# Kernel tuning notes

Hardware: AMD Instinct MI355X
Metric: run time of the kernel (lower is better)

## Reference

```python
import jax, jax.numpy as jnp
import numpy as np

D = 1536; H = 12; DH = 128; B = 1; S_TXT = 512; S_IMG = 1024; S = S_TXT + S_IMG; FF = 4 * D
EPS = 1e-6


def setup_inputs() -> dict:
    key = jax.random.key(0)
    ks = iter(jax.random.split(key, 64))
    def nrm(shape, s=1.0):
        return jax.random.normal(next(ks), shape, jnp.float32) * s
    w = 0.02
    inp = {}
    inp["hidden_states"] = nrm((B, S_IMG, D))
    inp["encoder_hidden_states"] = nrm((B, S_TXT, D))
    inp["temb"] = nrm((B, D))
    ang = jax.random.uniform(next(ks), (B, S, DH // 2), jnp.float32, 0.0, 2.0 * np.pi)
    c, s = jnp.cos(ang), jnp.sin(ang)
    rot = jnp.stack([jnp.stack([c, -s], -1), jnp.stack([s, c], -1)], -2)  # [B,S,DH/2,2,2]
    inp["image_rotary_emb"] = rot.reshape(1, 1, B * S, DH // 2, 2, 2)
    inp["adaln_img_w"] = nrm((D, 6 * D), w); inp["adaln_img_b"] = jnp.zeros((6 * D,), jnp.float32)
    inp["adaln_txt_w"] = nrm((D, 6 * D), w); inp["adaln_txt_b"] = jnp.zeros((6 * D,), jnp.float32)
    inp["qkv_img_w"] = nrm((D, 3 * D), w); inp["qkv_img_b"] = jnp.zeros((3 * D,), jnp.float32)
    inp["qkv_txt_w"] = nrm((D, 3 * D), w); inp["qkv_txt_b"] = jnp.zeros((3 * D,), jnp.float32)
    inp["q_norm_img"] = jnp.ones((DH,), jnp.float32); inp["k_norm_img"] = jnp.ones((DH,), jnp.float32)
    inp["q_norm_txt"] = jnp.ones((DH,), jnp.float32); inp["k_norm_txt"] = jnp.ones((DH,), jnp.float32)
    inp["out_img_w"] = nrm((D, D), w); inp["out_img_b"] = jnp.zeros((D,), jnp.float32)
    inp["out_txt_w"] = nrm((D, D), w); inp["out_txt_b"] = jnp.zeros((D,), jnp.float32)
    inp["mlp_img_w1"] = nrm((D, FF), w); inp["mlp_img_b1"] = jnp.zeros((FF,), jnp.float32)
    inp["mlp_img_w2"] = nrm((FF, D), w); inp["mlp_img_b2"] = jnp.zeros((D,), jnp.float32)
    inp["mlp_txt_w1"] = nrm((D, FF), w); inp["mlp_txt_b1"] = jnp.zeros((FF,), jnp.float32)
    inp["mlp_txt_w2"] = nrm((FF, D), w); inp["mlp_txt_b2"] = jnp.zeros((D,), jnp.float32)
    return inp


def _ln(x):  # LayerNorm, no affine
    m = jnp.mean(x, -1, keepdims=True)
    v = jnp.mean(jnp.square(x - m), -1, keepdims=True)
    return (x - m) * jax.lax.rsqrt(v + EPS)


def _rms(x, w):  # per-head RMSNorm
    return x * jax.lax.rsqrt(jnp.mean(jnp.square(x), -1, keepdims=True) + EPS) * w


def _rope(x, rot):  # x [B,H,S,DH], rot [B,S,DH/2,2,2]
    xp = x.reshape(*x.shape[:-1], DH // 2, 2)
    out = jnp.einsum('bsdij,bhsdj->bhsdi', rot, xp)
    return out.reshape(x.shape)


def _qkv(x, w, b, qn, kn):  # -> q,k,v each [B,H,S,DH]
    bb, ss, _ = x.shape
    qkv = (x @ w + b).reshape(bb, ss, 3, H, DH).transpose(2, 0, 3, 1, 4)
    q, k, v = qkv[0], qkv[1], qkv[2]
    return _rms(q, qn), _rms(k, kn), v


def _block(hidden_states, encoder_hidden_states, temb, rot,
           adaln_img_w, adaln_img_b, adaln_txt_w, adaln_txt_b,
           qkv_img_w, qkv_img_b, qkv_txt_w, qkv_txt_b,
           q_norm_img, k_norm_img, q_norm_txt, k_norm_txt,
           out_img_w, out_img_b, out_txt_w, out_txt_b,
           mlp_img_w1, mlp_img_b1, mlp_img_w2, mlp_img_b2,
           mlp_txt_w1, mlp_txt_b1, mlp_txt_w2, mlp_txt_b2):
    bsz = hidden_states.shape[0]
    s_txt = encoder_hidden_states.shape[1]
    t = jax.nn.silu(temb)
    emb_i = t @ adaln_img_w + adaln_img_b
    emb_t = t @ adaln_txt_w + adaln_txt_b
    sh_i, sc_i, g_i, shm_i, scm_i, gm_i = [e[:, None, :] for e in jnp.split(emb_i, 6, -1)]
    sh_t, sc_t, g_t, shm_t, scm_t, gm_t = [e[:, None, :] for e in jnp.split(emb_t, 6, -1)]

    n_img = _ln(hidden_states) * (1.0 + sc_i) + sh_i
    n_txt = _ln(encoder_hidden_states) * (1.0 + sc_t) + sh_t

    qi, ki, vi = _qkv(n_img, qkv_img_w, qkv_img_b, q_norm_img, k_norm_img)
    qt, kt, vt = _qkv(n_txt, qkv_txt_w, qkv_txt_b, q_norm_txt, k_norm_txt)
    q = jnp.concatenate([qt, qi], axis=2)
    k = jnp.concatenate([kt, ki], axis=2)
    v = jnp.concatenate([vt, vi], axis=2)

    rot = rot.reshape(bsz, q.shape[2], DH // 2, 2, 2)
    q = _rope(q, rot)
    k = _rope(k, rot)

    scale = 1.0 / np.sqrt(DH)
    attn = jax.nn.softmax(jnp.einsum('bhqd,bhkd->bhqk', q, k) * scale, axis=-1)
    o = jnp.einsum('bhqk,bhkd->bhqd', attn, v)          # [B,H,S,DH]
    o = o.transpose(0, 2, 1, 3).reshape(bsz, -1, D)     # [B,S,D]
    a_txt, a_img = o[:, :s_txt], o[:, s_txt:]

    hidden_states = hidden_states + g_i * (a_img @ out_img_w + out_img_b)
    encoder_hidden_states = encoder_hidden_states + g_t * (a_txt @ out_txt_w + out_txt_b)

    n2_img = _ln(hidden_states) * (1.0 + scm_i) + shm_i
    ff_img = jax.nn.gelu(n2_img @ mlp_img_w1 + mlp_img_b1, approximate=True) @ mlp_img_w2 + mlp_img_b2
    hidden_states = hidden_states + gm_i * ff_img

    n2_txt = _ln(encoder_hidden_states) * (1.0 + scm_t) + shm_t
    ff_txt = jax.nn.gelu(n2_txt @ mlp_txt_w1 + mlp_txt_b1, approximate=True) @ mlp_txt_w2 + mlp_txt_b2
    encoder_hidden_states = encoder_hidden_states + gm_t * ff_txt

    return jnp.concatenate([encoder_hidden_states, hidden_states], axis=1)


def reference(hidden_states, encoder_hidden_states, temb, image_rotary_emb,
              adaln_img_w, adaln_img_b, adaln_txt_w, adaln_txt_b,
              qkv_img_w, qkv_img_b, qkv_txt_w, qkv_txt_b,
              q_norm_img, k_norm_img, q_norm_txt, k_norm_txt,
              out_img_w, out_img_b, out_txt_w, out_txt_b,
              mlp_img_w1, mlp_img_b1, mlp_img_w2, mlp_img_b2,
              mlp_txt_w1, mlp_txt_b1, mlp_txt_w2, mlp_txt_b2):
    s_txt = encoder_hidden_states.shape[1]
    out = _block(hidden_states, encoder_hidden_states, temb, image_rotary_emb,
                 adaln_img_w, adaln_img_b, adaln_txt_w, adaln_txt_b,
                 qkv_img_w, qkv_img_b, qkv_txt_w, qkv_txt_b,
                 q_norm_img, k_norm_img, q_norm_txt, k_norm_txt,
                 out_img_w, out_img_b, out_txt_w, out_txt_b,
                 mlp_img_w1, mlp_img_b1, mlp_img_w2, mlp_img_b2,
                 mlp_txt_w1, mlp_txt_b1, mlp_txt_w2, mlp_txt_b2)
    return (out[:, :s_txt], out[:, s_txt:])
```

## Files before the change

kernel.cpp:

```cpp
#include <hip/hip_runtime.h>
#include <hip/hip_bf16.h>

typedef __bf16 bf16_t;
typedef __attribute__((ext_vector_type(4))) float f32x4;
typedef __attribute__((ext_vector_type(8))) bf16_t bf16x8;
typedef __attribute__((ext_vector_type(4))) bf16_t bf16x4;
typedef __attribute__((ext_vector_type(2))) bf16_t bf16x2;

#define D_MODEL 1536
#define NH 12
#define DHD 128
#define S_TXT 512
#define S_TOT 1536
#define FF_DIM 6144
#define KVSPLIT 4
#define HQB 288

__device__ inline bf16x8 ld_frag(const bf16_t* p) {
    bf16x4 a = *(const bf16x4*)p;
    bf16x4 b = *(const bf16x4*)(p + 16);
    bf16x8 r;
    r[0]=a[0]; r[1]=a[1]; r[2]=a[2]; r[3]=a[3];
    r[4]=b[0]; r[5]=b[1]; r[6]=b[2]; r[7]=b[3];
    return r;
}

__device__ inline void gload16(const void* g, void* l) {
    __builtin_amdgcn_global_load_lds((const __attribute__((address_space(1))) unsigned int*)g,
                                     (__attribute__((address_space(3))) unsigned int*)l, 16, 0, 0);
}

__global__ __launch_bounds__(256)
void adaln_p(const float* __restrict__ temb,
             const float* __restrict__ w_img, const float* __restrict__ w_txt,
             float* __restrict__ part) {
    __shared__ float t[192];
    int tid = threadIdx.x;
    int k0 = blockIdx.y * 192;
    if (tid < 192) {
        float x = temb[k0 + tid];
        t[tid] = x / (1.0f + __expf(-x));
    }
    __syncthreads();
    int n_g = blockIdx.x * 256 + tid;
    bool img = n_g < 9216;
    const float* W = img ? w_img : w_txt;
    int n = img ? n_g : n_g - 9216;
    float acc = 0.f;
    for (int kk = 0; kk < 192; kk += 4) {
        acc += t[kk]     * W[(size_t)(k0 + kk) * 9216 + n];
        acc += t[kk + 1] * W[(size_t)(k0 + kk + 1) * 9216 + n];
        acc += t[kk + 2] * W[(size_t)(k0 + kk + 2) * 9216 + n];
        acc += t[kk + 3] * W[(size_t)(k0 + kk + 3) * 9216 + n];
    }
    part[(size_t)blockIdx.y * 18432 + n_g] = acc;
}

__global__ __launch_bounds__(256)
void adaln_r(const float* __restrict__ part,
             const float* __restrict__ b_img, const float* __restrict__ b_txt,
             float* __restrict__ emb_img, float* __restrict__ emb_txt) {
    int n_g = blockIdx.x * 256 + threadIdx.x;
    float a = 0.f;
#pragma unroll
    for (int kc = 0; kc < 8; ++kc) a += part[(size_t)kc * 18432 + n_g];
    if (n_g < 9216) emb_img[n_g] = a + b_img[n_g];
    else            emb_txt[n_g - 9216] = a + b_txt[n_g - 9216];
}

__global__ __launch_bounds__(256)
void ln_mod(const float* __restrict__ src_txt, const float* __restrict__ src_img,
            const float* __restrict__ emb_t, const float* __restrict__ emb_i,
            int sh_c, int sc_c, bf16_t* __restrict__ out) {
    int row = blockIdx.x;
    bool txt = row < S_TXT;
    const float* src = txt ? src_txt + (size_t)row * D_MODEL
                           : src_img + (size_t)(row - S_TXT) * D_MODEL;
    const float* emb = txt ? emb_t : emb_i;
    int tid = threadIdx.x;
    float2 v[3];
    float s = 0.f, sq = 0.f;
#pragma unroll
    for (int i = 0; i < 3; ++i) {
        v[i] = *(const float2*)(src + tid * 2 + 512 * i);
        s  += v[i].x + v[i].y;
        sq += v[i].x * v[i].x + v[i].y * v[i].y;
    }
#pragma unroll
    for (int off = 32; off > 0; off >>= 1) {
        s  += __shfl_down(s, off);
        sq += __shfl_down(sq, off);
    }
    __shared__ float red[8];
    int wave = tid >> 6, lane = tid & 63;
    if (lane == 0) { red[wave] = s; red[4 + wave] = sq; }
    __syncthreads();
    float ts = red[0] + red[1] + red[2] + red[3];
    float tq = red[4] + red[5] + red[6] + red[7];
    float mean = ts * (1.0f / D_MODEL);
    float var  = tq * (1.0f / D_MODEL) - mean * mean;
    float rstd = rsqrtf(var + 1e-6f);
    bf16_t* op = out + (size_t)row * D_MODEL;
#pragma unroll
    for (int i = 0; i < 3; ++i) {
        int c0 = tid * 2 + 512 * i;
        bf16x2 r;
        r[0] = (bf16_t)((v[i].x - mean) * rstd * (1.0f + emb[sc_c * D_MODEL + c0])     + emb[sh_c * D_MODEL + c0]);
        r[1] = (bf16_t)((v[i].y - mean) * rstd * (1.0f + emb[sc_c * D_MODEL + c0 + 1]) + emb[sh_c * D_MODEL + c0 + 1]);
        *(bf16x2*)(op + c0) = r;
    }
}

template <int K, int N>
__global__ __launch_bounds__(256)
void conv_wt(const float* __restrict__ w_t, const float* __restrict__ w_i,
             bf16_t* __restrict__ dst) {
    __shared__ float tile[64][65];
    const float* src = blockIdx.z ? w_i : w_t;
    bf16_t* d = dst + (size_t)blockIdx.z * N * K;
    int bn = blockIdx.x * 64, bk = blockIdx.y * 64;
    int tid = threadIdx.x;
#pragma unroll
    for (int j = 0; j < 16; ++j) {
        int l = tid + 256 * j;
        int k = l >> 6, n = l & 63;
        tile[k][n] = src[(size_t)(bk + k) * N + bn + n];
    }
    __syncthreads();
#pragma unroll
    for (int j = 0; j < 16; ++j) {
        int l = tid + 256 * j;
        int n = l >> 6, k = l & 63;
        d[(size_t)(bn + n) * K + bk + k] = (bf16_t)tile[k][n];
    }
}

template <int EPI, typename OutT>
__global__ __launch_bounds__(256)
void gemm2(const bf16_t* __restrict__ A, int lda,
           const bf16_t* __restrict__ Wt, int wimg_off,
           const float* __restrict__ bias_t, const float* __restrict__ bias_i,
           const float* __restrict__ resid_t, const float* __restrict__ resid_i, int ldr,
           const float* __restrict__ gate_t, const float* __restrict__ gate_i,
           OutT* __restrict__ out, int ldo, int K) {
    __shared__ bf16_t As[2][128 * 64];
    __shared__ bf16_t Bs[2][128 * 64];
    const int tid = threadIdx.x;

    const int nbx = gridDim.x;
    const int nwg = nbx * gridDim.y;
    int lb = blockIdx.y * nbx + blockIdx.x;
    if ((nwg & 7) == 0) lb = (lb & 7) * (nwg >> 3) + (lb >> 3);
    const int bm = (lb / nbx) * 128, bn = (lb % nbx) * 128;

    const bool txt = bm < S_TXT;
    const bf16_t* W = txt ? Wt : Wt + wimg_off;
    const float* bias = txt ? bias_t : bias_i;
    const int wave = tid >> 6, lane = tid & 63;
    const int wr = (wave >> 1) * 64, wc = (wave & 1) * 64;
    const int lr = lane & 15, lg = lane >> 4;

    const int srow = wave * 8 + (lane >> 3);
    const int csrc = ((lane & 7) ^ ((lane >> 3) & 7)) * 8;
    const bf16_t* Ab = A + (size_t)(bm + srow) * lda + csrc;
    const bf16_t* Wb = W + (size_t)(bn + srow) * K + csrc;
    const int ldst = (wave * 8) * 64;

    f32x4 acc[4][4] = {};
    const int nt = K >> 6;

    auto stage = [&](int buf, int t) {
#pragma unroll
        for (int j = 0; j < 4; ++j) {
            gload16(Ab + (size_t)j * 32 * lda + t * 64, &As[buf][ldst + j * 2048]);
            gload16(Wb + (size_t)j * 32 * K   + t * 64, &Bs[buf][ldst + j * 2048]);
        }
    };

    stage(0, 0);
    asm volatile("s_waitcnt vmcnt(0)" ::: "memory");
    __builtin_amdgcn_s_barrier();

    int cur = 0;
    for (int t = 0; t < nt; ++t) {
        if (t + 1 < nt) stage(cur ^ 1, t + 1);
#pragma unroll
        for (int kk = 0; kk < 2; ++kk) {
            bf16x8 af[4], bfm[4];
#pragma unroll
            for (int m = 0; m < 4; ++m) {
                int rr = wr + m * 16 + lr;
                af[m] = *(const bf16x8*)&As[cur][rr * 64 + (((kk * 4 + lg) ^ (lr & 7)) * 8)];
            }
#pragma unroll
            for (int n = 0; n < 4; ++n) {
                int rr = wc + n * 16 + lr;
                bfm[n] = *(const bf16x8*)&Bs[cur][rr * 64 + (((kk * 4 + lg) ^ (lr & 7)) * 8)];
            }
#pragma unroll
            for (int m = 0; m < 4; ++m)
#pragma unroll
                for (int n = 0; n < 4; ++n)
                    acc[m][n] = __builtin_amdgcn_mfma_f32_16x16x32_bf16(af[m], bfm[n], acc[m][n], 0, 0, 0);
        }
        asm volatile("s_waitcnt vmcnt(0)" ::: "memory");
        __builtin_amdgcn_s_barrier();
        cur ^= 1;
    }

    const float* gate  = txt ? gate_t : gate_i;
    const float* resid = txt ? resid_t : resid_i;
    const int rbase = txt ? 0 : S_TXT;
#pragma unroll
    for (int m = 0; m < 4; ++m) {
#pragma unroll
        for (int r = 0; r < 4; ++r) {
            int grow = bm + wr + m * 16 + lg * 4 + r;
#pragma unroll
            for (int n = 0; n < 4; ++n) {
                int gcol = bn + wc + n * 16 + lr;
                float v = acc[m][n][r] + bias[gcol];
                if constexpr (EPI == 1) {
                    float x = v;
                    float th = tanhf(0.7978845608028654f * (x + 0.044715f * x * x * x));
                    v = 0.5f * x * (1.0f + th);
                } else if constexpr (EPI == 2) {
                    v = resid[(size_t)(grow - rbase) * ldr + gcol] + gate[gcol] * v;
                }
                out[(size_t)grow * ldo + gcol] = (OutT)v;
            }
        }
    }
}

__global__ __launch_bounds__(256)
void gemm3(const bf16_t* __restrict__ A, int lda,
           const bf16_t* __restrict__ Wt, int wimg_off,
           const float* __restrict__ bias_t, const float* __restrict__ bias_i,
           const float* __restrict__ resid_t, const float* __restrict__ resid_i, int ldr,
           const float* __restrict__ gate_t, const float* __restrict__ gate_i,
           float* __restrict__ out, int ldo, int K) {
    __shared__ bf16_t As[2][128 * 64];
    __shared__ bf16_t Bs[2][64 * 64];
    const int tid = threadIdx.x;

    const int nbx = gridDim.x;
    const int nwg = nbx * gridDim.y;
    int lb = blockIdx.y * nbx + blockIdx.x;
    if ((nwg & 7) == 0) lb = (lb & 7) * (nwg >> 3) + (lb >> 3);
    const int bm = (lb / nbx) * 128, bn = (lb % nbx) * 64;

    const bool txt = bm < S_TXT;
    const bf16_t* W = txt ? Wt : Wt + wimg_off;
    const float* bias = txt ? bias_t : bias_i;
    const int wave = tid >> 6, lane = tid & 63;
    const int wr = (wave >> 1) * 64, wc = (wave & 1) * 32;
    const int lr = lane & 15, lg = lane >> 4;

    const int srow = wave * 8 + (lane >> 3);
    const int csrc = ((lane & 7) ^ ((lane >> 3) & 7)) * 8;
    const bf16_t* Ab = A + (size_t)(bm + srow) * lda + csrc;
    const bf16_t* Wb = W + (size_t)(bn + srow) * K + csrc;
    const int ldst = (wave * 8) * 64;

    f32x4 acc[4][2] = {};
    const int nt = K >> 6;

    auto stage = [&](int buf, int t) {
#pragma unroll
        for (int j = 0; j < 4; ++j)
            gload16(Ab + (size_t)j * 32 * lda + t * 64, &As[buf][ldst + j * 2048]);
#pragma unroll
        for (int j = 0; j < 2; ++j)
            gload16(Wb + (size_t)j * 32 * K + t * 64, &Bs[buf][ldst + j * 2048]);
    };

    stage(0, 0);
    asm volatile("s_waitcnt vmcnt(0)" ::: "memory");
    __builtin_amdgcn_s_barrier();

    int cur = 0;
    for (int t = 0; t < nt; ++t) {
        if (t + 1 < nt) stage(cur ^ 1, t + 1);
#pragma unroll
        for (int kk = 0; kk < 2; ++kk) {
            bf16x8 af[4], bfm[2];
#pragma unroll
            for (int m = 0; m < 4; ++m) {
                int rr = wr + m * 16 + lr;
                af[m] = *(const bf16x8*)&As[cur][rr * 64 + (((kk * 4 + lg) ^ (lr & 7)) * 8)];
            }
#pragma unroll
            for (int n = 0; n < 2; ++n) {
                int rr = wc + n * 16 + lr;
                bfm[n] = *(const bf16x8*)&Bs[cur][rr * 64 + (((kk * 4 + lg) ^ (lr & 7)) * 8)];
            }
#pragma unroll
            for (int m = 0; m < 4; ++m)
#pragma unroll
                for (int n = 0; n < 2; ++n)
                    acc[m][n] = __builtin_amdgcn_mfma_f32_16x16x32_bf16(af[m], bfm[n], acc[m][n], 0, 0, 0);
        }
        asm volatile("s_waitcnt vmcnt(0)" ::: "memory");
        __builtin_amdgcn_s_barrier();
        cur ^= 1;
    }

    const float* gate  = txt ? gate_t : gate_i;
    const float* resid = txt ? resid_t : resid_i;
    const int rbase = txt ? 0 : S_TXT;
#pragma unroll
    for (int m = 0; m < 4; ++m) {
#pragma unroll
        for (int r = 0; r < 4; ++r) {
            int grow = bm + wr + m * 16 + lg * 4 + r;
#pragma unroll
            for (int n = 0; n < 2; ++n) {
                int gcol = bn + wc + n * 16 + lr;
                float v = acc[m][n][r] + bias[gcol];
                v = resid[(size_t)(grow - rbase) * ldr + gcol] + gate[gcol] * v;
                out[(size_t)grow * ldo + gcol] = v;
            }
        }
    }
}

__global__ __launch_bounds__(128)
void qkv_epi(const bf16_t* __restrict__ qkv, const float* __restrict__ rope,
             const float* __restrict__ qn_i, const float* __restrict__ kn_i,
             const float* __restrict__ qn_t, const float* __restrict__ kn_t,
             bf16_t* __restrict__ qb, bf16_t* __restrict__ kb) {
    int h = blockIdx.x, s = blockIdx.y, dh = threadIdx.x;
    bool txt = s < S_TXT;
    const float* qn = txt ? qn_t : qn_i;
    const float* kn = txt ? kn_t : kn_i;
    const bf16_t* base = qkv + (size_t)s * 4608 + h * DHD + dh;
    float q = (float)base[0];
    float k = (float)base[D_MODEL];
    float qs = q * q, ks = k * k;
#pragma unroll
    for (int off = 32; off > 0; off >>= 1) {
        qs += __shfl_down(qs, off);
        ks += __shfl_down(ks, off);
    }
    __shared__ float red[4];
    if ((threadIdx.x & 63) == 0) {
        red[(threadIdx.x >> 6) * 2]     = qs;
        red[(threadIdx.x >> 6) * 2 + 1] = ks;
    }
    __syncthreads();
    float qr = rsqrtf((red[0] + red[2]) * (1.0f / DHD) + 1e-6f);
    float kr = rsqrtf((red[1] + red[3]) * (1.0f / DHD) + 1e-6f);
    q = q * qr * qn[dh];
    k = k * kr * kn[dh];
    int i = dh & 1, d = dh >> 1;
    const float* rp = rope + ((size_t)s * 64 + d) * 4 + i * 2;
    float r0 = rp[0], r1 = rp[1];
    float qo = __shfl_xor(q, 1), ko = __shfl_xor(k, 1);
    float q0 = i ? qo : q, q1 = i ? q : qo;
    float k0 = i ? ko : k, k1 = i ? k : ko;
    float qq = r0 * q0 + r1 * q1;
    float kk = r0 * k0 + r1 * k1;
    size_t idx = ((size_t)h * S_TOT + s) * DHD + dh;
    qb[idx] = (bf16_t)(qq * 0.08838834764831845f);
    kb[idx] = (bf16_t)kk;
}

__global__ __launch_bounds__(256)
void v_tr(const bf16_t* __restrict__ qkv, bf16_t* __restrict__ vt) {
    __shared__ bf16_t tile[64][130];
    int h = blockIdx.x, sb = blockIdx.y * 64;
    int tid = threadIdx.x;
#pragma unroll
    for (int j = 0; j < 32; ++j) {
        int linear = tid + 256 * j;
        int sl = linear >> 7, dh = linear & 127;
        tile[sl][dh] = qkv[(size_t)(sb + sl) * 4608 + 2 * D_MODEL + h * DHD + dh];
    }
    __syncthreads();
#pragma unroll
    for (int j = 0; j < 32; ++j) {
        int linear = tid + 256 * j;
        int dh = linear >> 6, sl = linear & 63;
        vt[((size_t)h * DHD + dh) * S_TOT + sb + sl] = tile[sl][dh];
    }
}

__global__ __launch_bounds__(256)
void attn_k(const bf16_t* __restrict__ qbuf, const bf16_t* __restrict__ kbuf,
            const bf16_t* __restrict__ vt,
            float* __restrict__ part_o, float* __restrict__ part_ml) {
    __shared__ bf16_t Ks[2][64 * 128];
    __shared__ bf16_t Vs[2][128 * 64];
    __shared__ bf16_t P[4][16 * 64];
    int h = blockIdx.x, qblk = blockIdx.y, z = blockIdx.z;
    int q0 = qblk * 64;
    int tid = threadIdx.x, wave = tid >> 6, lane = tid & 63;
    int lr = lane & 15, lg = lane >> 4;

    const bf16_t* Qp = qbuf + ((size_t)h * S_TOT + q0 + wave * 16 + lr) * DHD;
    bf16x8 qf[4];
#pragma unroll
    for (int kk = 0; kk < 4; ++kk) qf[kk] = *(const bf16x8*)(Qp + (kk * 4 + lg) * 8);

    const int sKr = wave * 4 + (lane >> 4);
    const int cK = lane & 15;
    const bf16_t* Kb = kbuf + ((size_t)h * S_TOT + sKr) * DHD + ((cK ^ (sKr & 7)) * 8);
    const int ldsK = sKr * 128 - (lane >> 4) * 128 + 0;
    const int sVr = wave * 8 + (lane >> 3);
    const int cV = lane & 7;
    const bf16_t* Vb = vt + ((size_t)h * DHD + sVr) * S_TOT + ((cV ^ (sVr & 7)) * 8);
    const int ldsV = (wave * 8) * 64;

    auto stage = [&](int buf, int kb0) {
#pragma unroll
        for (int j = 0; j < 4; ++j) {
            gload16(Kb + (size_t)(kb0 + j * 16) * DHD, &Ks[buf][(wave * 4) * 128 + j * 2048]);
            gload16(Vb + kb0 + (size_t)j * 32 * S_TOT, &Vs[buf][ldsV + j * 2048]);
        }
    };

    f32x4 of[8] = {};
    float m[4] = {-1e30f, -1e30f, -1e30f, -1e30f};
    float l[4] = {};
    const int kv0 = z * (S_TOT / KVSPLIT);
    const int nt = (S_TOT / KVSPLIT) / 64;

    stage(0, kv0);
    asm volatile("s_waitcnt vmcnt(0)" ::: "memory");
    __builtin_amdgcn_s_barrier();

    int cur = 0;
    for (int t = 0; t < nt; ++t) {
        if (t + 1 < nt) stage(cur ^ 1, kv0 + (t + 1) * 64);
        f32x4 sf[4] = {};
        __builtin_amdgcn_s_setprio(1);
#pragma unroll
        for (int n = 0; n < 4; ++n) {
#pragma unroll
            for (int kk = 0; kk < 4; ++kk) {
                bf16x8 kf = *(const bf16x8*)&Ks[cur][(n * 16 + lr) * 128 + (((kk * 4 + lg) ^ (lr & 7)) * 8)];
                sf[n] = __builtin_amdgcn_mfma_f32_16x16x32_bf16(qf[kk], kf, sf[n], 0, 0, 0);
            }
        }
        __builtin_amdgcn_s_setprio(0);
        float bm[4], alpha[4], rs[4];
#pragma unroll
        for (int r = 0; r < 4; ++r)
            bm[r] = fmaxf(fmaxf(sf[0][r], sf[1][r]), fmaxf(sf[2][r], sf[3][r]));
#pragma unroll
        for (int mask = 1; mask < 16; mask <<= 1)
#pragma unroll
            for (int r = 0; r < 4; ++r) bm[r] = fmaxf(bm[r], __shfl_xor(bm[r], mask));
#pragma unroll
        for (int r = 0; r < 4; ++r) {
            float mn = fmaxf(m[r], bm[r]);
            alpha[r] = __expf(m[r] - mn);
            m[r] = mn;
            rs[r] = 0.f;
        }
#pragma unroll
        for (int n = 0; n < 4; ++n)
#pragma unroll
            for (int r = 0; r < 4; ++r) {
                float p = __expf(sf[n][r] - m[r]);
                rs[r] += p;
                int row = lg * 4 + r, col = n * 16 + lr;
                P[wave][row * 64 + ((((col >> 3) ^ (row & 7)) << 3) | (col & 7))] = (bf16_t)p;
            }
#pragma unroll
        for (int mask = 1; mask < 16; mask <<= 1)
#pragma unroll
            for (int r = 0; r < 4; ++r) rs[r] += __shfl_xor(rs[r], mask);
#pragma unroll
        for (int r = 0; r < 4; ++r) l[r] = l[r] * alpha[r] + rs[r];
#pragma unroll
        for (int nf = 0; nf < 8; ++nf)
#pragma unroll
            for (int r = 0; r < 4; ++r) of[nf][r] *= alpha[r];
        __builtin_amdgcn_s_setprio(1);
#pragma unroll
        for (int kk2 = 0; kk2 < 2; ++kk2) {
            bf16x8 pf = *(const bf16x8*)&P[wave][lr * 64 + (((kk2 * 4 + lg) ^ (lr & 7)) * 8)];
#pragma unroll
            for (int nf = 0; nf < 8; ++nf) {
                bf16x8 vf = *(const bf16x8*)&Vs[cur][(nf * 16 + lr) * 64 + (((kk2 * 4 + lg) ^ (lr & 7)) * 8)];
                of[nf] = __builtin_amdgcn_mfma_f32_16x16x32_bf16(pf, vf, of[nf], 0, 0, 0);
            }
        }
        __builtin_amdgcn_s_setprio(0);
        asm volatile("s_waitcnt vmcnt(0)" ::: "memory");
        __builtin_amdgcn_s_barrier();
        cur ^= 1;
    }
    int hqb = h * 24 + qblk;
    float* po = part_o + ((size_t)z * HQB + hqb) * 8192;
    int rb = wave * 16 + lg * 4;
#pragma unroll
    for (int r = 0; r < 4; ++r)
#pragma unroll
        for (int nf = 0; nf < 8; ++nf)
            po[(rb + r) * 128 + nf * 16 + lr] = of[nf][r];
    if (lr == 0) {
#pragma unroll
        for (int r = 0; r < 4; ++r) {
            size_t mi = (((size_t)z * HQB + hqb) * 64 + rb + r) * 2;
            part_ml[mi]     = m[r];
            part_ml[mi + 1] = l[r];
        }
    }
}

__global__ __launch_bounds__(256)
void attn_red(const float* __restrict__ part_o, const float* __restrict__ part_ml,
              bf16_t* __restrict__ o) {
    int hqb = blockIdx.x;
    int h = hqb / 24, q0 = (hqb % 24) * 64;
    __shared__ float wz[KVSPLIT][64];
    __shared__ float invL[64];
    int tid = threadIdx.x;
    if (tid < 64) {
        float mz[KVSPLIT], lz[KVSPLIT];
#pragma unroll
        for (int zz = 0; zz < KVSPLIT; ++zz) {
            size_t mi = (((size_t)zz * HQB + hqb) * 64 + tid) * 2;
            mz[zz] = part_ml[mi];
            lz[zz] = part_ml[mi + 1];
        }
        float M = mz[0];
#pragma unroll
        for (int zz = 1; zz < KVSPLIT; ++zz) M = fmaxf(M, mz[zz]);
        float L = 0.f;
#pragma unroll
        for (int zz = 0; zz < KVSPLIT; ++zz) {
            float w = __expf(mz[zz] - M);
            wz[zz][tid] = w;
            L += w * lz[zz];
        }
        invL[tid] = 1.0f / L;
    }
    __syncthreads();
#pragma unroll
    for (int i = 0; i < 8; ++i) {
        int e4 = tid + 256 * i;
        int row = e4 >> 5, c4 = e4 & 31;
        f32x4 acc = {};
#pragma unroll
        for (int zz = 0; zz < KVSPLIT; ++zz) {
            f32x4 v = *(const f32x4*)&part_o[((size_t)zz * HQB + hqb) * 8192 + row * 128 + c4 * 4];
            float w = wz[zz][row];
            acc[0] += v[0] * w; acc[1] += v[1] * w; acc[2] += v[2] * w; acc[3] += v[3] * w;
        }
        float il = invL[row];
        bf16x4 r;
        r[0] = (bf16_t)(acc[0] * il); r[1] = (bf16_t)(acc[1] * il);
        r[2] = (bf16_t)(acc[2] * il); r[3] = (bf16_t)(acc[3] * il);
        *(bf16x4*)&o[(size_t)(q0 + row) * D_MODEL + h * DHD + c4 * 4] = r;
    }
}

extern "C" void kernel_launch(void* const* d_in, const int* in_sizes, int n_in,
                              void* d_out, int out_size, void* d_ws, size_t ws_size,
                              hipStream_t stream) {
    const float* hidden  = (const float*)d_in[0];
    const float* encoder = (const float*)d_in[1];
    const float* temb    = (const float*)d_in[2];
    const float* rope    = (const float*)d_in[3];
    const float* adaln_img_w = (const float*)d_in[4];
    const float* adaln_img_b = (const float*)d_in[5];
    const float* adaln_txt_w = (const float*)d_in[6];
    const float* adaln_txt_b = (const float*)d_in[7];
    const float* qkv_img_w = (const float*)d_in[8];
    const float* qkv_img_b = (const float*)d_in[9];
    const float* qkv_txt_w = (const float*)d_in[10];
    const float* qkv_txt_b = (const float*)d_in[11];
    const float* qn_img = (const float*)d_in[12];
    const float* kn_img = (const float*)d_in[13];
    const float* qn_txt = (const float*)d_in[14];
    const float* kn_txt = (const float*)d_in[15];
    const float* out_img_w = (const float*)d_in[16];
    const float* out_img_b = (const float*)d_in[17];
    const float* out_txt_w = (const float*)d_in[18];
    const float* out_txt_b = (const float*)d_in[19];
    const float* mlp_img_w1 = (const float*)d_in[20];
    const float* mlp_img_b1 = (const float*)d_in[21];
    const float* mlp_img_w2 = (const float*)d_in[22];
    const float* mlp_img_b2 = (const float*)d_in[23];
    const float* mlp_txt_w1 = (const float*)d_in[24];
    const float* mlp_txt_b1 = (const float*)d_in[25];
    const float* mlp_txt_w2 = (const float*)d_in[26];
    const float* mlp_txt_b2 = (const float*)d_in[27];
    float* dout = (float*)d_out;
    char* wsb = (char*)d_ws;

    float*  emb_i = (float*)(wsb);
    float*  emb_t = (float*)(wsb + 36864);
    bf16_t* wreg  = (bf16_t*)(wsb + 73728);
    float*  part  = (float*)(wsb + 73728);
    float*  part_o = (float*)(wsb + 73728);
    bf16_t* n1    = (bf16_t*)(wsb + 37822464);
    float*  part_ml = (float*)(wsb + 37822464);
    bf16_t* qkvb  = (bf16_t*)(wsb + 42541056);
    bf16_t* obuf  = qkvb;
    bf16_t* ffb   = qkvb + 2359296;
    bf16_t* qb    = (bf16_t*)(wsb + 56696832);
    bf16_t* kb    = (bf16_t*)(wsb + 61415424);
    bf16_t* vt    = (bf16_t*)(wsb + 66134016);

    adaln_p<<<dim3(72, 8), 256, 0, stream>>>(temb, adaln_img_w, adaln_txt_w, part);
    adaln_r<<<72, 256, 0, stream>>>(part, adaln_img_b, adaln_txt_b, emb_i, emb_t);
    ln_mod<<<S_TOT, 256, 0, stream>>>(encoder, hidden, emb_t, emb_i, 0, 1, n1);
    conv_wt<1536, 4608><<<dim3(72, 24, 2), 256, 0, stream>>>(qkv_txt_w, qkv_img_w, wreg);
    gemm2<0, bf16_t><<<dim3(36, 12), 256, 0, stream>>>(
        n1, D_MODEL, wreg, 4608 * 1536, qkv_txt_b, qkv_img_b,
        nullptr, nullptr, 0, nullptr, nullptr, qkvb, 4608, 1536);
    qkv_epi<<<dim3(12, 1536), 128, 0, stream>>>(qkvb, rope, qn_img, kn_img, qn_txt, kn_txt, qb, kb);
    v_tr<<<dim3(12, 24), 256, 0, stream>>>(qkvb, vt);
    attn_k<<<dim3(12, 24, KVSPLIT), 256, 0, stream>>>(qb, kb, vt, part_o, part_ml);
    attn_red<<<HQB, 256, 0, stream>>>(part_o, part_ml, obuf);
    conv_wt<1536, 1536><<<dim3(24, 24, 2), 256, 0, stream>>>(out_txt_w, out_img_w, wreg);
    gemm3<<<dim3(24, 12), 256, 0, stream>>>(
        obuf, D_MODEL, wreg, 1536 * 1536, out_txt_b, out_img_b,
        encoder, hidden, D_MODEL, emb_t + 2 * D_MODEL, emb_i + 2 * D_MODEL,
        dout, D_MODEL, 1536);
    ln_mod<<<S_TOT, 256, 0, stream>>>(dout, dout + (size_t)S_TXT * D_MODEL, emb_t, emb_i, 3, 4, n1);
    conv_wt<1536, 6144><<<dim3(96, 24, 2), 256, 0, stream>>>(mlp_txt_w1, mlp_img_w1, wreg);
    gemm2<1, bf16_t><<<dim3(48, 12), 256, 0, stream>>>(
        n1, D_MODEL, wreg, 6144 * 1536, mlp_txt_b1, mlp_img_b1,
        nullptr, nullptr, 0, nullptr, nullptr, ffb, FF_DIM, 1536);
    conv_wt<6144, 1536><<<dim3(24, 96, 2), 256, 0, stream>>>(mlp_txt_w2, mlp_img_w2, wreg);
    gemm3<<<dim3(24, 12), 256, 0, stream>>>(
        ffb, FF_DIM, wreg, 1536 * 6144, mlp_txt_b2, mlp_img_b2,
        dout, dout + (size_t)S_TXT * D_MODEL, D_MODEL,
        emb_t + 5 * D_MODEL, emb_i + 5 * D_MODEL, dout, D_MODEL, 6144);
    (void)in_sizes; (void)n_in; (void)out_size; (void)ws_size;
}
```

Before: 394.1 us.

## Use 256x128 tiles with 512 threads and triple-buffered GEMM pipelines

Replaces the 128x128 gemm2 with gemm4, which uses 256x128 tiles, 8 waves and a three-stage LDS buffer. Global-to-LDS loads are issued two tiles ahead and split across the two k-halves, and the wait drops from vmcnt(0) to a partial vmcnt. The aim is to hide global load latency behind MFMA work. gemm3 gets the same triple buffering and s_setprio around its MFMA blocks. The cost is more LDS per block (gemm4 uses 144KB) and fewer workgroups, so occupancy and wave quantization may suffer.

```diff
diff --git a/kernel.cpp b/kernel.cpp
--- a/kernel.cpp
+++ b/kernel.cpp
@@ -15,15 +15,6 @@
 #define FF_DIM 6144
 #define KVSPLIT 4
 #define HQB 288
-
-__device__ inline bf16x8 ld_frag(const bf16_t* p) {
-    bf16x4 a = *(const bf16x4*)p;
-    bf16x4 b = *(const bf16x4*)(p + 16);
-    bf16x8 r;
-    r[0]=a[0]; r[1]=a[1]; r[2]=a[2]; r[3]=a[3];
-    r[4]=b[0]; r[5]=b[1]; r[6]=b[2]; r[7]=b[3];
-    return r;
-}
 
 __device__ inline void gload16(const void* g, void* l) {
     __builtin_amdgcn_global_load_lds((const __attribute__((address_space(1))) unsigned int*)g,
@@ -135,99 +126,118 @@
     }
 }
 
-template <int EPI, typename OutT>
-__global__ __launch_bounds__(256)
-void gemm2(const bf16_t* __restrict__ A, int lda,
+template <int EPI>
+__global__ __launch_bounds__(512)
+void gemm4(const bf16_t* __restrict__ A, int lda,
            const bf16_t* __restrict__ Wt, int wimg_off,
            const float* __restrict__ bias_t, const float* __restrict__ bias_i,
-           const float* __restrict__ resid_t, const float* __restrict__ resid_i, int ldr,
-           const float* __restrict__ gate_t, const float* __restrict__ gate_i,
-           OutT* __restrict__ out, int ldo, int K) {
-    __shared__ bf16_t As[2][128 * 64];
-    __shared__ bf16_t Bs[2][128 * 64];
+           bf16_t* __restrict__ out, int ldo, int K) {
+    __shared__ bf16_t As[3][256 * 64];
+    __shared__ bf16_t Bs[3][128 * 64];
     const int tid = threadIdx.x;
 
     const int nbx = gridDim.x;
     const int nwg = nbx * gridDim.y;
     int lb = blockIdx.y * nbx + blockIdx.x;
-    if ((nwg & 7) == 0) lb = (lb & 7) * (nwg >> 3) + (lb >> 3);
-    const int bm = (lb / nbx) * 128, bn = (lb % nbx) * 128;
+    lb = (lb & 7) * (nwg >> 3) + (lb >> 3);
+    const int bm = (lb / nbx) * 256, bn = (lb % nbx) * 128;
 
     const bool txt = bm < S_TXT;
     const bf16_t* W = txt ? Wt : Wt + wimg_off;
     const float* bias = txt ? bias_t : bias_i;
-    const int wave = tid >> 6, lane = tid & 63;
-    const int wr = (wave >> 1) * 64, wc = (wave & 1) * 64;
+
+    const int wid = tid >> 6, lane = tid & 63;
+    const int wm = wid >> 1, wn = wid & 1;
     const int lr = lane & 15, lg = lane >> 4;
 
-    const int srow = wave * 8 + (lane >> 3);
+    const int srow = tid >> 3;
     const int csrc = ((lane & 7) ^ ((lane >> 3) & 7)) * 8;
     const bf16_t* Ab = A + (size_t)(bm + srow) * lda + csrc;
     const bf16_t* Wb = W + (size_t)(bn + srow) * K + csrc;
-    const int ldst = (wave * 8) * 64;
+    const int ldsbase = (wid * 8) * 64;
 
     f32x4 acc[4][4] = {};
     const int nt = K >> 6;
 
-    auto stage = [&](int buf, int t) {
-#pragma unroll
-        for (int j = 0; j < 4; ++j) {
-            gload16(Ab + (size_t)j * 32 * lda + t * 64, &As[buf][ldst + j * 2048]);
-            gload16(Wb + (size_t)j * 32 * K   + t * 64, &Bs[buf][ldst + j * 2048]);
-        }
+    auto loadA = [&](int buf, int t, int j) {
+        gload16(Ab + (size_t)(j * 64) * lda + t * 64, &As[buf][ldsbase + j * 4096]);
     };
-
-    stage(0, 0);
-    asm volatile("s_waitcnt vmcnt(0)" ::: "memory");
+    auto loadB = [&](int buf, int t, int j) {
+        gload16(Wb + (size_t)(j * 64) * K + t * 64, &Bs[buf][ldsbase + j * 4096]);
+    };
+
+#pragma unroll
+    for (int j = 0; j < 4; ++j) loadA(0, 0, j);
+#pragma unroll
+    for (int j = 0; j < 2; ++j) loadB(0, 0, j);
+#pragma unroll
+    for (int j = 0; j < 4; ++j) loadA(1, 1, j);
+#pragma unroll
+    for (int j = 0; j < 2; ++j) loadB(1, 1, j);
+    asm volatile("s_waitcnt vmcnt(6)" ::: "memory");
     __builtin_amdgcn_s_barrier();
 
-    int cur = 0;
+    int buf = 0;
     for (int t = 0; t < nt; ++t) {
-        if (t + 1 < nt) stage(cur ^ 1, t + 1);
-#pragma unroll
-        for (int kk = 0; kk < 2; ++kk) {
-            bf16x8 af[4], bfm[4];
-#pragma unroll
-            for (int m = 0; m < 4; ++m) {
-                int rr = wr + m * 16 + lr;
-                af[m] = *(const bf16x8*)&As[cur][rr * 64 + (((kk * 4 + lg) ^ (lr & 7)) * 8)];
-            }
+        const int nbuf = (buf == 0) ? 2 : buf - 1;
+        const bool pre = (t + 2) < nt;
+        if (pre) { loadA(nbuf, t + 2, 0); loadA(nbuf, t + 2, 1); loadA(nbuf, t + 2, 2); }
+        {
+            bf16x8 af[4], bfr[4];
+#pragma unroll
+            for (int m = 0; m < 4; ++m)
+                af[m] = *(const bf16x8*)&As[buf][(wm * 64 + m * 16 + lr) * 64 + ((lg ^ (lr & 7)) * 8)];
+#pragma unroll
+            for (int n = 0; n < 4; ++n)
+                bfr[n] = *(const bf16x8*)&Bs[buf][(wn * 64 + n * 16 + lr) * 64 + ((lg ^ (lr & 7)) * 8)];
+            __builtin_amdgcn_s_setprio(1);
+#pragma unroll
+            for (int m = 0; m < 4; ++m)
+#pragma unroll
+                for (int n = 0; n < 4; ++n)
+                    acc[m][n] = __builtin_amdgcn_mfma_f32_16x16x32_bf16(af[m], bfr[n], acc[m][n], 0, 0, 0);
+            __builtin_amdgcn_s_setprio(0);
+        }
+        if (pre) { loadA(nbuf, t + 2, 3); loadB(nbuf, t + 2, 0); loadB(nbuf, t + 2, 1); }
+        {
+            bf16x8 af[4], bfr[4];
+#pragma unroll
+            for (int m = 0; m < 4; ++m)
+                af[m] = *(const bf16x8*)&As[buf][(wm * 64 + m * 16 + lr) * 64 + (((4 + lg) ^ (lr & 7)) * 8)];
+#pragma unroll
+            for (int n = 0; n < 4; ++n)
+                bfr[n] = *(const bf16x8*)&Bs[buf][(wn * 64 + n * 16 + lr) * 64 + (((4 + lg) ^ (lr & 7)) * 8)];
+            __builtin_amdgcn_s_setprio(1);
+#pragma unroll
+            for (int m = 0; m < 4; ++m)
+#pragma unroll
+                for (int n = 0; n < 4; ++n)
+                    acc[m][n] = __builtin_amdgcn_mfma_f32_16x16x32_bf16(af[m], bfr[n], acc[m][n], 0, 0, 0);
+            __builtin_amdgcn_s_setprio(0);
+        }
+        if (t + 1 < nt) {
+            if (pre) asm volatile("s_waitcnt vmcnt(6)" ::: "memory");
+            else     asm volatile("s_waitcnt vmcnt(0)" ::: "memory");
+            __builtin_amdgcn_s_barrier();
+        }
+        buf = (buf == 2) ? 0 : buf + 1;
+    }
+
+#pragma unroll
+    for (int m = 0; m < 4; ++m) {
+#pragma unroll
+        for (int r = 0; r < 4; ++r) {
+            int grow = bm + wm * 64 + m * 16 + lg * 4 + r;
 #pragma unroll
             for (int n = 0; n < 4; ++n) {
-                int rr = wc + n * 16 + lr;
-                bfm[n] = *(const bf16x8*)&Bs[cur][rr * 64 + (((kk * 4 + lg) ^ (lr & 7)) * 8)];
-            }
-#pragma unroll
-            for (int m = 0; m < 4; ++m)
-#pragma unroll
-                for (int n = 0; n < 4; ++n)
-                    acc[m][n] = __builtin_amdgcn_mfma_f32_16x16x32_bf16(af[m], bfm[n], acc[m][n], 0, 0, 0);
-        }
-        asm volatile("s_waitcnt vmcnt(0)" ::: "memory");
-        __builtin_amdgcn_s_barrier();
-        cur ^= 1;
-    }
-
-    const float* gate  = txt ? gate_t : gate_i;
-    const float* resid = txt ? resid_t : resid_i;
-    const int rbase = txt ? 0 : S_TXT;
-#pragma unroll
-    for (int m = 0; m < 4; ++m) {
-#pragma unroll
-        for (int r = 0; r < 4; ++r) {
-            int grow = bm + wr + m * 16 + lg * 4 + r;
-#pragma unroll
-            for (int n = 0; n < 4; ++n) {
-                int gcol = bn + wc + n * 16 + lr;
+                int gcol = bn + wn * 64 + n * 16 + lr;
                 float v = acc[m][n][r] + bias[gcol];
                 if constexpr (EPI == 1) {
                     float x = v;
                     float th = tanhf(0.7978845608028654f * (x + 0.044715f * x * x * x));
                     v = 0.5f * x * (1.0f + th);
-                } else if constexpr (EPI == 2) {
-                    v = resid[(size_t)(grow - rbase) * ldr + gcol] + gate[gcol] * v;
                 }
-                out[(size_t)grow * ldo + gcol] = (OutT)v;
+                out[(size_t)grow * ldo + gcol] = (bf16_t)v;
             }
         }
     }
@@ -240,8 +250,8 @@
            const float* __restrict__ resid_t, const float* __restrict__ resid_i, int ldr,
            const float* __restrict__ gate_t, const float* __restrict__ gate_i,
            float* __restrict__ out, int ldo, int K) {
-    __shared__ bf16_t As[2][128 * 64];
-    __shared__ bf16_t Bs[2][64 * 64];
+    __shared__ bf16_t As[3][128 * 64];
+    __shared__ bf16_t Bs[3][64 * 64];
     const int tid = threadIdx.x;
 
     const int nbx = gridDim.x;
@@ -257,7 +267,7 @@
     const int wr = (wave >> 1) * 64, wc = (wave & 1) * 32;
     const int lr = lane & 15, lg = lane >> 4;
 
-    const int srow = wave * 8 + (lane >> 3);
+    const int srow = tid >> 3;
     const int csrc = ((lane & 7) ^ ((lane >> 3) & 7)) * 8;
     const bf16_t* Ab = A + (size_t)(bm + srow) * lda + csrc;
     const bf16_t* Wb = W + (size_t)(bn + srow) * K + csrc;
@@ -266,44 +276,59 @@
     f32x4 acc[4][2] = {};
     const int nt = K >> 6;
 
-    auto stage = [&](int buf, int t) {
-#pragma unroll
-        for (int j = 0; j < 4; ++j)
-            gload16(Ab + (size_t)j * 32 * lda + t * 64, &As[buf][ldst + j * 2048]);
-#pragma unroll
-        for (int j = 0; j < 2; ++j)
-            gload16(Wb + (size_t)j * 32 * K + t * 64, &Bs[buf][ldst + j * 2048]);
+    auto loadA = [&](int buf, int t, int j) {
+        gload16(Ab + (size_t)(j * 32) * lda + t * 64, &As[buf][ldst + j * 2048]);
     };
-
-    stage(0, 0);
-    asm volatile("s_waitcnt vmcnt(0)" ::: "memory");
+    auto loadB = [&](int buf, int t, int j) {
+        gload16(Wb + (size_t)(j * 32) * K + t * 64, &Bs[buf][ldst + j * 2048]);
+    };
+
+#pragma unroll
+    for (int j = 0; j < 4; ++j) loadA(0, 0, j);
+#pragma unroll
+    for (int j = 0; j < 2; ++j) loadB(0, 0, j);
+#pragma unroll
+    for (int j = 0; j < 4; ++j) loadA(1, 1, j);
+#pragma unroll
+    for (int j = 0; j < 2; ++j) loadB(1, 1, j);
+    asm volatile("s_waitcnt vmcnt(6)" ::: "memory");
     __builtin_amdgcn_s_barrier();
 
-    int cur = 0;
+    int buf = 0;
     for (int t = 0; t < nt; ++t) {
-        if (t + 1 < nt) stage(cur ^ 1, t + 1);
+        const int nbuf = (buf == 0) ? 2 : buf - 1;
+        const bool pre = (t + 2) < nt;
 #pragma unroll
         for (int kk = 0; kk < 2; ++kk) {
+            if (pre) {
+                if (kk == 0) { loadA(nbuf, t + 2, 0); loadA(nbuf, t + 2, 1); loadA(nbuf, t + 2, 2); }
+                else         { loadA(nbuf, t + 2, 3); loadB(nbuf, t + 2, 0); loadB(nbuf, t + 2, 1); }
+            }
             bf16x8 af[4], bfm[2];
 #pragma unroll
             for (int m = 0; m < 4; ++m) {
                 int rr = wr + m * 16 + lr;
-                af[m] = *(const bf16x8*)&As[cur][rr * 64 + (((kk * 4 + lg) ^ (lr & 7)) * 8)];
+                af[m] = *(const bf16x8*)&As[buf][rr * 64 + (((kk * 4 + lg) ^ (lr & 7)) * 8)];
             }
 #pragma unroll
             for (int n = 0; n < 2; ++n) {
                 int rr = wc + n * 16 + lr;
-                bfm[n] = *(const bf16x8*)&Bs[cur][rr * 64 + (((kk * 4 + lg) ^ (lr & 7)) * 8)];
-            }
+                bfm[n] = *(const bf16x8*)&Bs[buf][rr * 64 + (((kk * 4 + lg) ^ (lr & 7)) * 8)];
+            }
+            __builtin_amdgcn_s_setprio(1);
 #pragma unroll
             for (int m = 0; m < 4; ++m)
 #pragma unroll
                 for (int n = 0; n < 2; ++n)
                     acc[m][n] = __builtin_amdgcn_mfma_f32_16x16x32_bf16(af[m], bfm[n], acc[m][n], 0, 0, 0);
-        }
-        asm volatile("s_waitcnt vmcnt(0)" ::: "memory");
-        __builtin_amdgcn_s_barrier();
-        cur ^= 1;
+            __builtin_amdgcn_s_setprio(0);
+        }
+        if (t + 1 < nt) {
+            if (pre) asm volatile("s_waitcnt vmcnt(6)" ::: "memory");
+            else     asm volatile("s_waitcnt vmcnt(0)" ::: "memory");
+            __builtin_amdgcn_s_barrier();
+        }
+        buf = (buf == 2) ? 0 : buf + 1;
     }
 
     const float* gate  = txt ? gate_t : gate_i;
@@ -406,7 +431,6 @@
     const int sKr = wave * 4 + (lane >> 4);
     const int cK = lane & 15;
     const bf16_t* Kb = kbuf + ((size_t)h * S_TOT + sKr) * DHD + ((cK ^ (sKr & 7)) * 8);
-    const int ldsK = sKr * 128 - (lane >> 4) * 128 + 0;
     const int sVr = wave * 8 + (lane >> 3);
     const int cV = lane & 7;
     const bf16_t* Vb = vt + ((size_t)h * DHD + sVr) * S_TOT + ((cV ^ (sVr & 7)) * 8);
@@ -611,9 +635,8 @@
     adaln_r<<<72, 256, 0, stream>>>(part, adaln_img_b, adaln_txt_b, emb_i, emb_t);
     ln_mod<<<S_TOT, 256, 0, stream>>>(encoder, hidden, emb_t, emb_i, 0, 1, n1);
     conv_wt<1536, 4608><<<dim3(72, 24, 2), 256, 0, stream>>>(qkv_txt_w, qkv_img_w, wreg);
-    gemm2<0, bf16_t><<<dim3(36, 12), 256, 0, stream>>>(
-        n1, D_MODEL, wreg, 4608 * 1536, qkv_txt_b, qkv_img_b,
-        nullptr, nullptr, 0, nullptr, nullptr, qkvb, 4608, 1536);
+    gemm4<0><<<dim3(36, 6), 512, 0, stream>>>(
+        n1, D_MODEL, wreg, 4608 * 1536, qkv_txt_b, qkv_img_b, qkvb, 4608, 1536);
     qkv_epi<<<dim3(12, 1536), 128, 0, stream>>>(qkvb, rope, qn_img, kn_img, qn_txt, kn_txt, qb, kb);
     v_tr<<<dim3(12, 24), 256, 0, stream>>>(qkvb, vt);
     attn_k<<<dim3(12, 24, KVSPLIT), 256, 0, stream>>>(qb, kb, vt, part_o, part_ml);
@@ -625,9 +648,8 @@
         dout, D_MODEL, 1536);
     ln_mod<<<S_TOT, 256, 0, stream>>>(dout, dout + (size_t)S_TXT * D_MODEL, emb_t, emb_i, 3, 4, n1);
     conv_wt<1536, 6144><<<dim3(96, 24, 2), 256, 0, stream>>>(mlp_txt_w1, mlp_img_w1, wreg);
-    gemm2<1, bf16_t><<<dim3(48, 12), 256, 0, stream>>>(
-        n1, D_MODEL, wreg, 6144 * 1536, mlp_txt_b1, mlp_img_b1,
-        nullptr, nullptr, 0, nullptr, nullptr, ffb, FF_DIM, 1536);
+    gemm4<1><<<dim3(48, 6), 512, 0, stream>>>(
+        n1, D_MODEL, wreg, 6144 * 1536, mlp_txt_b1, mlp_img_b1, ffb, FF_DIM, 1536);
     conv_wt<6144, 1536><<<dim3(24, 96, 2), 256, 0, stream>>>(mlp_txt_w2, mlp_img_w2, wreg);
     gemm3<<<dim3(24, 12), 256, 0, stream>>>(
         ffb, FF_DIM, wreg, 1536 * 6144, mlp_txt_b2, mlp_img_b2,
```

New measurement: 462.0 us. +17.2%, slower.

## Replace 128x128 GEMM with 256x256 eight-wave pipelined GEMM for QKV and MLP1

Applied to the files above, without the earlier changes.

Introduces a 256x256 tile GEMM with 512 threads and 8 waves that splits each k-step into four quadrant phases. Loads for the next tile are interleaved between phases, with partial vmcnt waits and MFMA priority raises. The aim is higher data reuse per LDS byte and better overlap of global loads with MFMA work. The grid shrinks to 108/144 workgroups, fewer than the CUs available, and each block uses a large LDS footprint.

```diff
diff --git a/kernel.cpp b/kernel.cpp
--- a/kernel.cpp
+++ b/kernel.cpp
@@ -15,15 +15,6 @@
 #define FF_DIM 6144
 #define KVSPLIT 4
 #define HQB 288
-
-__device__ inline bf16x8 ld_frag(const bf16_t* p) {
-    bf16x4 a = *(const bf16x4*)p;
-    bf16x4 b = *(const bf16x4*)(p + 16);
-    bf16x8 r;
-    r[0]=a[0]; r[1]=a[1]; r[2]=a[2]; r[3]=a[3];
-    r[4]=b[0]; r[5]=b[1]; r[6]=b[2]; r[7]=b[3];
-    return r;
-}
 
 __device__ inline void gload16(const void* g, void* l) {
     __builtin_amdgcn_global_load_lds((const __attribute__((address_space(1))) unsigned int*)g,
@@ -135,99 +126,115 @@
     }
 }
 
-template <int EPI, typename OutT>
-__global__ __launch_bounds__(256)
-void gemm2(const bf16_t* __restrict__ A, int lda,
+template <int EPI>
+__global__ __launch_bounds__(512)
+void gemm5(const bf16_t* __restrict__ A, int lda,
            const bf16_t* __restrict__ Wt, int wimg_off,
            const float* __restrict__ bias_t, const float* __restrict__ bias_i,
-           const float* __restrict__ resid_t, const float* __restrict__ resid_i, int ldr,
-           const float* __restrict__ gate_t, const float* __restrict__ gate_i,
-           OutT* __restrict__ out, int ldo, int K) {
-    __shared__ bf16_t As[2][128 * 64];
-    __shared__ bf16_t Bs[2][128 * 64];
+           bf16_t* __restrict__ out, int ldo, int K) {
+    __shared__ bf16_t As[2][256 * 64];
+    __shared__ bf16_t Bs[2][256 * 64];
     const int tid = threadIdx.x;
 
     const int nbx = gridDim.x;
     const int nwg = nbx * gridDim.y;
     int lb = blockIdx.y * nbx + blockIdx.x;
-    if ((nwg & 7) == 0) lb = (lb & 7) * (nwg >> 3) + (lb >> 3);
-    const int bm = (lb / nbx) * 128, bn = (lb % nbx) * 128;
+    {
+        int q = nwg >> 3, r = nwg & 7, x = lb & 7, o = lb >> 3;
+        lb = (x < r ? x * (q + 1) : r * (q + 1) + (x - r) * q) + o;
+    }
+    const int bm = (lb / nbx) * 256, bn = (lb % nbx) * 256;
 
     const bool txt = bm < S_TXT;
     const bf16_t* W = txt ? Wt : Wt + wimg_off;
     const float* bias = txt ? bias_t : bias_i;
-    const int wave = tid >> 6, lane = tid & 63;
-    const int wr = (wave >> 1) * 64, wc = (wave & 1) * 64;
+
+    const int wid = tid >> 6, lane = tid & 63;
+    const int wm = wid >> 2, wn = wid & 3;
     const int lr = lane & 15, lg = lane >> 4;
 
-    const int srow = wave * 8 + (lane >> 3);
+    const int srow = tid >> 3;
     const int csrc = ((lane & 7) ^ ((lane >> 3) & 7)) * 8;
     const bf16_t* Ab = A + (size_t)(bm + srow) * lda + csrc;
     const bf16_t* Wb = W + (size_t)(bn + srow) * K + csrc;
-    const int ldst = (wave * 8) * 64;
-
-    f32x4 acc[4][4] = {};
+
+    auto stA = [&](int buf, int t, int j) {
+        gload16(Ab + (size_t)(j * 64) * lda + t * 64, &As[buf][j * 4096 + wid * 512]);
+    };
+    auto stB = [&](int buf, int t, int j) {
+        gload16(Wb + (size_t)(j * 64) * K + t * 64, &Bs[buf][j * 4096 + wid * 512]);
+    };
+
+    f32x4 acc[8][4] = {};
     const int nt = K >> 6;
 
-    auto stage = [&](int buf, int t) {
-#pragma unroll
-        for (int j = 0; j < 4; ++j) {
-            gload16(Ab + (size_t)j * 32 * lda + t * 64, &As[buf][ldst + j * 2048]);
-            gload16(Wb + (size_t)j * 32 * K   + t * 64, &Bs[buf][ldst + j * 2048]);
-        }
-    };
-
-    stage(0, 0);
-    asm volatile("s_waitcnt vmcnt(0)" ::: "memory");
-    __builtin_amdgcn_s_barrier();
-
-    int cur = 0;
+    stA(0, 0, 0); stA(0, 0, 1);
+    stB(0, 0, 0); stB(0, 0, 1);
+    stA(0, 0, 2); stA(0, 0, 3);
+    stB(0, 0, 2); stB(0, 0, 3);
+
+#define G5_PHASE(QM, QN)                                                                     \
+    {                                                                                        \
+        bf16x8 af[4][2], bfr[2][2];                                                          \
+        _Pragma("unroll") for (int m = 0; m < 4; ++m) {                                      \
+            int rr = (QM) * 128 + wm * 64 + m * 16 + lr;                                     \
+            _Pragma("unroll") for (int kk = 0; kk < 2; ++kk)                                 \
+                af[m][kk] = *(const bf16x8*)&As[cur][rr * 64 + (((kk * 4 + lg) ^ (lr & 7)) * 8)]; \
+        }                                                                                    \
+        _Pragma("unroll") for (int n = 0; n < 2; ++n) {                                      \
+            int rr = (QN) * 128 + wn * 32 + n * 16 + lr;                                     \
+            _Pragma("unroll") for (int kk = 0; kk < 2; ++kk)                                 \
+                bfr[n][kk] = *(const bf16x8*)&Bs[cur][rr * 64 + (((kk * 4 + lg) ^ (lr & 7)) * 8)]; \
+        }                                                                                    \
+        __builtin_amdgcn_s_setprio(1);                                                       \
+        _Pragma("unroll") for (int m = 0; m < 4; ++m)                                        \
+            _Pragma("unroll") for (int n = 0; n < 2; ++n)                                    \
+                _Pragma("unroll") for (int kk = 0; kk < 2; ++kk)                             \
+                    acc[(QM) * 4 + m][(QN) * 2 + n] = __builtin_amdgcn_mfma_f32_16x16x32_bf16( \
+                        af[m][kk], bfr[n][kk], acc[(QM) * 4 + m][(QN) * 2 + n], 0, 0, 0);     \
+        __builtin_amdgcn_s_setprio(0);                                                       \
+    }
+
     for (int t = 0; t < nt; ++t) {
-        if (t + 1 < nt) stage(cur ^ 1, t + 1);
-#pragma unroll
-        for (int kk = 0; kk < 2; ++kk) {
-            bf16x8 af[4], bfm[4];
-#pragma unroll
-            for (int m = 0; m < 4; ++m) {
-                int rr = wr + m * 16 + lr;
-                af[m] = *(const bf16x8*)&As[cur][rr * 64 + (((kk * 4 + lg) ^ (lr & 7)) * 8)];
-            }
-#pragma unroll
-            for (int n = 0; n < 4; ++n) {
-                int rr = wc + n * 16 + lr;
-                bfm[n] = *(const bf16x8*)&Bs[cur][rr * 64 + (((kk * 4 + lg) ^ (lr & 7)) * 8)];
-            }
-#pragma unroll
-            for (int m = 0; m < 4; ++m)
-#pragma unroll
-                for (int n = 0; n < 4; ++n)
-                    acc[m][n] = __builtin_amdgcn_mfma_f32_16x16x32_bf16(af[m], bfm[n], acc[m][n], 0, 0, 0);
-        }
-        asm volatile("s_waitcnt vmcnt(0)" ::: "memory");
+        const int cur = t & 1, nxt = cur ^ 1;
+        const bool pre = (t + 1 < nt);
+        asm volatile("s_waitcnt vmcnt(4)" ::: "memory");
         __builtin_amdgcn_s_barrier();
-        cur ^= 1;
-    }
-
-    const float* gate  = txt ? gate_t : gate_i;
-    const float* resid = txt ? resid_t : resid_i;
-    const int rbase = txt ? 0 : S_TXT;
-#pragma unroll
-    for (int m = 0; m < 4; ++m) {
+        if (pre) { stA(nxt, t + 1, 0); stA(nxt, t + 1, 1); }
+        G5_PHASE(0, 0)
+        if (pre) asm volatile("s_waitcnt vmcnt(4)" ::: "memory");
+        else     asm volatile("s_waitcnt vmcnt(2)" ::: "memory");
+        __builtin_amdgcn_s_barrier();
+        if (pre) { stB(nxt, t + 1, 0); stB(nxt, t + 1, 1); }
+        G5_PHASE(1, 0)
+        if (pre) asm volatile("s_waitcnt vmcnt(4)" ::: "memory");
+        else     asm volatile("s_waitcnt vmcnt(0)" ::: "memory");
+        __builtin_amdgcn_s_barrier();
+        if (pre) { stA(nxt, t + 1, 2); stA(nxt, t + 1, 3); }
+        G5_PHASE(1, 1)
+        __builtin_amdgcn_s_barrier();
+        if (pre) { stB(nxt, t + 1, 2); stB(nxt, t + 1, 3); }
+        G5_PHASE(0, 1)
+    }
+#undef G5_PHASE
+
+#pragma unroll
+    for (int mf = 0; mf < 8; ++mf) {
+        int qm = mf >> 2, m = mf & 3;
 #pragma unroll
         for (int r = 0; r < 4; ++r) {
-            int grow = bm + wr + m * 16 + lg * 4 + r;
-#pragma unroll
-            for (int n = 0; n < 4; ++n) {
-                int gcol = bn + wc + n * 16 + lr;
-                float v = acc[m][n][r] + bias[gcol];
+            int grow = bm + qm * 128 + wm * 64 + m * 16 + lg * 4 + r;
+#pragma unroll
+            for (int nf = 0; nf < 4; ++nf) {
+                int qn = nf >> 1, n = nf & 1;
+                int gcol = bn + qn * 128 + wn * 32 + n * 16 + lr;
+                float v = acc[mf][nf][r] + bias[gcol];
                 if constexpr (EPI == 1) {
                     float x = v;
                     float th = tanhf(0.7978845608028654f * (x + 0.044715f * x * x * x));
                     v = 0.5f * x * (1.0f + th);
-                } else if constexpr (EPI == 2) {
-                    v = resid[(size_t)(grow - rbase) * ldr + gcol] + gate[gcol] * v;
                 }
-                out[(size_t)grow * ldo + gcol] = (OutT)v;
+                out[(size_t)grow * ldo + gcol] = (bf16_t)v;
             }
         }
     }
@@ -406,7 +413,6 @@
     const int sKr = wave * 4 + (lane >> 4);
     const int cK = lane & 15;
     const bf16_t* Kb = kbuf + ((size_t)h * S_TOT + sKr) * DHD + ((cK ^ (sKr & 7)) * 8);
-    const int ldsK = sKr * 128 - (lane >> 4) * 128 + 0;
     const int sVr = wave * 8 + (lane >> 3);
     const int cV = lane & 7;
     const bf16_t* Vb = vt + ((size_t)h * DHD + sVr) * S_TOT + ((cV ^ (sVr & 7)) * 8);
@@ -611,9 +617,8 @@
     adaln_r<<<72, 256, 0, stream>>>(part, adaln_img_b, adaln_txt_b, emb_i, emb_t);
     ln_mod<<<S_TOT, 256, 0, stream>>>(encoder, hidden, emb_t, emb_i, 0, 1, n1);
     conv_wt<1536, 4608><<<dim3(72, 24, 2), 256, 0, stream>>>(qkv_txt_w, qkv_img_w, wreg);
-    gemm2<0, bf16_t><<<dim3(36, 12), 256, 0, stream>>>(
-        n1, D_MODEL, wreg, 4608 * 1536, qkv_txt_b, qkv_img_b,
-        nullptr, nullptr, 0, nullptr, nullptr, qkvb, 4608, 1536);
+    gemm5<0><<<dim3(18, 6), 512, 0, stream>>>(
+        n1, D_MODEL, wreg, 4608 * 1536, qkv_txt_b, qkv_img_b, qkvb, 4608, 1536);
     qkv_epi<<<dim3(12, 1536), 128, 0, stream>>>(qkvb, rope, qn_img, kn_img, qn_txt, kn_txt, qb, kb);
     v_tr<<<dim3(12, 24), 256, 0, stream>>>(qkvb, vt);
     attn_k<<<dim3(12, 24, KVSPLIT), 256, 0, stream>>>(qb, kb, vt, part_o, part_ml);
@@ -625,9 +630,8 @@
         dout, D_MODEL, 1536);
     ln_mod<<<S_TOT, 256, 0, stream>>>(dout, dout + (size_t)S_TXT * D_MODEL, emb_t, emb_i, 3, 4, n1);
     conv_wt<1536, 6144><<<dim3(96, 24, 2), 256, 0, stream>>>(mlp_txt_w1, mlp_img_w1, wreg);
-    gemm2<1, bf16_t><<<dim3(48, 12), 256, 0, stream>>>(
-        n1, D_MODEL, wreg, 6144 * 1536, mlp_txt_b1, mlp_img_b1,
-        nullptr, nullptr, 0, nullptr, nullptr, ffb, FF_DIM, 1536);
+    gemm5<1><<<dim3(24, 6), 512, 0, stream>>>(
+        n1, D_MODEL, wreg, 6144 * 1536, mlp_txt_b1, mlp_img_b1, ffb, FF_DIM, 1536);
     conv_wt<6144, 1536><<<dim3(24, 96, 2), 256, 0, stream>>>(mlp_txt_w2, mlp_img_w2, wreg);
     gemm3<<<dim3(24, 12), 256, 0, stream>>>(
         ffb, FF_DIM, wreg, 1536 * 6144, mlp_txt_b2, mlp_img_b2,
```

Result: slower. 516.7 us (+31.1%).
